# Kernel optimization log

Hardware: AMD Instinct MI355X
Metric: run time of the kernel (lower is better)

The kernel has to match this reference:

```python
import jax, jax.numpy as jnp
import numpy as np

ALPHA = 0.15  # init kwarg alpha


def setup_inputs() -> dict:
    key = jax.random.key(0)
    k1, k2, k3, k4 = jax.random.split(key, 4)
    B, H, W, C = 16, 1024, 1024, 1
    I1 = jax.random.normal(k1, (B, H, W, C), jnp.float32)
    I2 = jax.random.normal(k2, (B, H, W, C), jnp.float32)
    u = jax.random.normal(k3, (B, H, W, C), jnp.float32)
    v = jax.random.normal(k4, (B, H, W, C), jnp.float32)
    return {"I1": I1, "I2": I2, "u": u, "v": v}


def _image_gradients(img):
    # Matches tf.image.image_gradients: returns (dy, dx), with last row/col zero.
    B, H, W, C = img.shape
    dy = jnp.concatenate([img[:, 1:, :, :] - img[:, :-1, :, :],
                          jnp.zeros((B, 1, W, C), img.dtype)], axis=1)
    dx = jnp.concatenate([img[:, :, 1:, :] - img[:, :, :-1, :],
                          jnp.zeros((B, H, 1, C), img.dtype)], axis=2)
    return dy, dx


def _warp(img, u, v):
    # Bilinear warp with zero padding at sample coords (x + 0.5*u, y + 0.5*v).
    # (The [-1,1] normalization + grid_sample align-corners denorm is identity.)
    B, H, W, C = img.shape
    x = jnp.arange(W, dtype=img.dtype)[None, None, :] + 0.5 * u[..., 0]  # (B,H,W)
    y = jnp.arange(H, dtype=img.dtype)[None, :, None] + 0.5 * v[..., 0]  # (B,H,W)
    x0 = jnp.floor(x)
    y0 = jnp.floor(y)
    x1 = x0 + 1.0
    y1 = y0 + 1.0
    wx1 = x - x0
    wx0 = 1.0 - wx1
    wy1 = y - y0
    wy0 = 1.0 - wy1
    img_flat = img.reshape(B, H * W, C)

    def gather(yi, xi):
        valid = (xi >= 0) & (xi <= W - 1) & (yi >= 0) & (yi <= H - 1)
        xi_c = jnp.clip(xi, 0, W - 1).astype(jnp.int32)
        yi_c = jnp.clip(yi, 0, H - 1).astype(jnp.int32)
        idx = (yi_c * W + xi_c).reshape(B, H * W, 1)
        vals = jnp.take_along_axis(img_flat, idx, axis=1).reshape(B, H, W, C)
        return vals * valid[..., None].astype(img.dtype)

    out = (gather(y0, x0) * (wy0 * wx0)[..., None]
           + gather(y0, x1) * (wy0 * wx1)[..., None]
           + gather(y1, x0) * (wy1 * wx0)[..., None]
           + gather(y1, x1) * (wy1 * wx1)[..., None])
    return out


def reference(I1, I2, u, v):
    # NOTE: faithful to the source, which assigns grad_x, grad_y = image_gradients(.)
    # even though tf.image.image_gradients returns (dy, dx).
    I1_grad_x, I1_grad_y = _image_gradients(I1)
    I1_warped = _warp(I1, u, v)
    dataTerm = I1_warped - I2
    u_next = u - ALPHA * dataTerm * I1_grad_x
    v_next = v - ALPHA * dataTerm * I1_grad_y
    return (u_next, v_next)
```

## Files before the change

### kernel.cpp

```cpp
#include <hip/hip_runtime.h>


#define ALPHA 0.15f
#define IMG_H 1024
#define IMG_W 1024
#define TW 128
#define TH 8
#define HALO 4
#define LW (TW + 9)
#define LH (TH + 9)

typedef float f32x4 __attribute__((ext_vector_type(4)));

__global__ __launch_bounds__(256) void dataterm_kernel(
        const float* __restrict__ I1,
        const float* __restrict__ I2,
        const float* __restrict__ u,
        const float* __restrict__ v,
        float* __restrict__ out_u,
        float* __restrict__ out_v) {
    const int W = IMG_W, H = IMG_H;
    const int t   = threadIdx.x;
    const int tx0 = blockIdx.x * TW;
    const int ty0 = blockIdx.y * TH;
    const int b   = blockIdx.z;

    const float* __restrict__ I1b = I1 + (size_t)b * (size_t)(H * W);

    __shared__ float S[LH * LW];

    for (int f = t; f < LH * LW; f += 256) {
        int ly = f / LW;
        int lx = f - ly * LW;
        int gy = min(max(ty0 - HALO + ly, 0), H - 1);
        int gx = min(max(tx0 - HALO + lx, 0), W - 1);
        S[f] = I1b[gy * W + gx];
    }
    __syncthreads();

    const int r  = t >> 5;
    const int cb = (t & 31) << 2;
    const int h  = ty0 + r;
    const int wb = tx0 + cb;
    const int p  = (b * H + h) * W + wb;

    f32x4 u4  = *(const f32x4*)(u + p);
    f32x4 v4  = *(const f32x4*)(v + p);
    f32x4 i24 = *(const f32x4*)(I2 + p);

    float uu[4] = { u4.x, u4.y, u4.z, u4.w };
    float vv[4] = { v4.x, v4.y, v4.z, v4.w };
    float i2[4] = { i24.x, i24.y, i24.z, i24.w };
    float ru[4], rv[4];

    const int cl = (HALO + r) * LW + HALO + cb;

    #pragma unroll
    for (int i = 0; i < 4; ++i) {
        float c     = S[cl + i];
        float right = S[cl + i + 1];
        float down  = S[cl + i + LW];
        float gxv = right - c;
        float gyv = down - c;

        float x = (float)(wb + i) + 0.5f * uu[i];
        float y = (float)h        + 0.5f * vv[i];

        float x0f = floorf(x);
        float y0f = floorf(y);
        float wx1 = x - x0f;
        float wx0 = 1.0f - wx1;
        float wy1 = y - y0f;
        float wy0 = 1.0f - wy1;

        int x0 = (int)x0f, y0 = (int)y0f;
        int x1 = x0 + 1,   y1 = y0 + 1;

        float vx0 = (x0 >= 0 && x0 <= W - 1) ? 1.0f : 0.0f;
        float vx1 = (x1 >= 0 && x1 <= W - 1) ? 1.0f : 0.0f;
        float vy0 = (y0 >= 0 && y0 <= H - 1) ? 1.0f : 0.0f;
        float vy1 = (y1 >= 0 && y1 <= H - 1) ? 1.0f : 0.0f;

        int lx0 = x0 - tx0 + HALO;
        int ly0 = y0 - ty0 + HALO;

        float g00, g01, g10, g11;
        if ((unsigned)lx0 <= (unsigned)(LW - 2) &&
            (unsigned)ly0 <= (unsigned)(LH - 2)) {
            int q = ly0 * LW + lx0;
            g00 = S[q]          * (vy0 * vx0);
            g01 = S[q + 1]      * (vy0 * vx1);
            g10 = S[q + LW]     * (vy1 * vx0);
            g11 = S[q + LW + 1] * (vy1 * vx1);
        } else {
            int x0c = min(max(x0, 0), W - 1);
            int x1c = min(max(x1, 0), W - 1);
            int y0c = min(max(y0, 0), H - 1);
            int y1c = min(max(y1, 0), H - 1);
            g00 = I1b[y0c * W + x0c] * (vy0 * vx0);
            g01 = I1b[y0c * W + x1c] * (vy0 * vx1);
            g10 = I1b[y1c * W + x0c] * (vy1 * vx0);
            g11 = I1b[y1c * W + x1c] * (vy1 * vx1);
        }

        float warped = g00 * (wy0 * wx0)
                     + g01 * (wy0 * wx1)
                     + g10 * (wy1 * wx0)
                     + g11 * (wy1 * wx1);

        float dataTerm = warped - i2[i];
        ru[i] = uu[i] - ALPHA * dataTerm * gyv;
        rv[i] = vv[i] - ALPHA * dataTerm * gxv;
    }

    f32x4 ruv = { ru[0], ru[1], ru[2], ru[3] };
    f32x4 rvv = { rv[0], rv[1], rv[2], rv[3] };
    __builtin_nontemporal_store(ruv, (f32x4*)(out_u + p));
    __builtin_nontemporal_store(rvv, (f32x4*)(out_v + p));
}

extern "C" void kernel_launch(void* const* d_in, const int* in_sizes, int n_in,
                              void* d_out, int out_size, void* d_ws, size_t ws_size,
                              hipStream_t stream) {
    const float* I1 = (const float*)d_in[0];
    const float* I2 = (const float*)d_in[1];
    const float* u  = (const float*)d_in[2];
    const float* v  = (const float*)d_in[3];

    int total = in_sizes[0];
    float* out_u = (float*)d_out;
    float* out_v = (float*)d_out + total;

    dim3 grid(IMG_W / TW, IMG_H / TH, total / (IMG_H * IMG_W));
    dataterm_kernel<<<grid, dim3(256), 0, stream>>>(I1, I2, u, v, out_u, out_v);
}
```

Measured before the change: 70.71 us.

## Double tile height, load halo via global_load_lds, prefetch streams before staging

Result: slower. 78.99 us (+11.7%).

```diff
diff --git a/kernel.cpp b/kernel.cpp
--- a/kernel.cpp
+++ b/kernel.cpp
@@ -5,10 +5,11 @@
 #define IMG_H 1024
 #define IMG_W 1024
 #define TW 128
-#define TH 8
+#define TH 16
 #define HALO 4
-#define LW (TW + 9)
-#define LH (TH + 9)
+#define LW 140
+#define LH 25
+#define LDS_N 3584
 
 typedef float f32x4 __attribute__((ext_vector_type(4)));
 
@@ -27,96 +28,113 @@
 
     const float* __restrict__ I1b = I1 + (size_t)b * (size_t)(H * W);
 
-    __shared__ float S[LH * LW];
+    __shared__ float S[LDS_N];
 
-    for (int f = t; f < LH * LW; f += 256) {
+    const int r  = t >> 5;
+    const int cb = (t & 31) << 2;
+    const int h0 = ty0 + r;
+    const int wb = tx0 + cb;
+    const int p0 = (b * H + h0) * W + wb;
+    const int p1 = p0 + 8 * W;
+
+    f32x4 u4a = *(const f32x4*)(u + p0);
+    f32x4 v4a = *(const f32x4*)(v + p0);
+    f32x4 i2a = *(const f32x4*)(I2 + p0);
+    f32x4 u4b = *(const f32x4*)(u + p1);
+    f32x4 v4b = *(const f32x4*)(v + p1);
+    f32x4 i2b = *(const f32x4*)(I2 + p1);
+
+    #pragma unroll
+    for (int j = 0; j < 14; ++j) {
+        int f  = t + 256 * j;
         int ly = f / LW;
         int lx = f - ly * LW;
-        int gy = min(max(ty0 - HALO + ly, 0), H - 1);
+        int gy = min(max(ty0 - HALO + min(ly, LH - 1), 0), H - 1);
         int gx = min(max(tx0 - HALO + lx, 0), W - 1);
-        S[f] = I1b[gy * W + gx];
+        __builtin_amdgcn_global_load_lds(
+            (const __attribute__((address_space(1))) void*)(I1b + gy * W + gx),
+            (__attribute__((address_space(3))) void*)(S + f), 4, 0, 0);
     }
     __syncthreads();
 
-    const int r  = t >> 5;
-    const int cb = (t & 31) << 2;
-    const int h  = ty0 + r;
-    const int wb = tx0 + cb;
-    const int p  = (b * H + h) * W + wb;
+    float ou[8], ov[8];
 
-    f32x4 u4  = *(const f32x4*)(u + p);
-    f32x4 v4  = *(const f32x4*)(v + p);
-    f32x4 i24 = *(const f32x4*)(I2 + p);
+    auto proc4 = [&](int h, int cl, const f32x4& u4, const f32x4& v4,
+                     const f32x4& i24, float* ru, float* rv) {
+        f32x4 c4 = *(const f32x4*)(S + cl);
+        f32x4 d4 = *(const f32x4*)(S + cl + LW);
+        float c4r = S[cl + 4];
+        float gyv[4] = { d4.x - c4.x, d4.y - c4.y, d4.z - c4.z, d4.w - c4.w };
+        float gxv[4] = { c4.y - c4.x, c4.z - c4.y, c4.w - c4.z, c4r - c4.w };
+        float uu[4] = { u4.x, u4.y, u4.z, u4.w };
+        float vv[4] = { v4.x, v4.y, v4.z, v4.w };
+        float i2[4] = { i24.x, i24.y, i24.z, i24.w };
 
-    float uu[4] = { u4.x, u4.y, u4.z, u4.w };
-    float vv[4] = { v4.x, v4.y, v4.z, v4.w };
-    float i2[4] = { i24.x, i24.y, i24.z, i24.w };
-    float ru[4], rv[4];
+        #pragma unroll
+        for (int i = 0; i < 4; ++i) {
+            float x = (float)(wb + i) + 0.5f * uu[i];
+            float y = (float)h        + 0.5f * vv[i];
 
-    const int cl = (HALO + r) * LW + HALO + cb;
+            float x0f = floorf(x);
+            float y0f = floorf(y);
+            float wx1 = x - x0f;
+            float wx0 = 1.0f - wx1;
+            float wy1 = y - y0f;
+            float wy0 = 1.0f - wy1;
 
-    #pragma unroll
-    for (int i = 0; i < 4; ++i) {
-        float c     = S[cl + i];
-        float right = S[cl + i + 1];
-        float down  = S[cl + i + LW];
-        float gxv = right - c;
-        float gyv = down - c;
+            int x0 = (int)x0f, y0 = (int)y0f;
+            int x1 = x0 + 1,   y1 = y0 + 1;
 
-        float x = (float)(wb + i) + 0.5f * uu[i];
-        float y = (float)h        + 0.5f * vv[i];
+            float vx0 = (x0 >= 0 && x0 <= W - 1) ? 1.0f : 0.0f;
+            float vx1 = (x1 >= 0 && x1 <= W - 1) ? 1.0f : 0.0f;
+            float vy0 = (y0 >= 0 && y0 <= H - 1) ? 1.0f : 0.0f;
+            float vy1 = (y1 >= 0 && y1 <= H - 1) ? 1.0f : 0.0f;
 
-        float x0f = floorf(x);
-        float y0f = floorf(y);
-        float wx1 = x - x0f;
-        float wx0 = 1.0f - wx1;
-        float wy1 = y - y0f;
-        float wy0 = 1.0f - wy1;
+            int lx0 = x0 - tx0 + HALO;
+            int ly0 = y0 - ty0 + HALO;
 
-        int x0 = (int)x0f, y0 = (int)y0f;
-        int x1 = x0 + 1,   y1 = y0 + 1;
+            float g00, g01, g10, g11;
+            if ((unsigned)lx0 <= (unsigned)(LW - 2) &&
+                (unsigned)ly0 <= (unsigned)(LH - 2)) {
+                int q = ly0 * LW + lx0;
+                g00 = S[q]          * (vy0 * vx0);
+                g01 = S[q + 1]      * (vy0 * vx1);
+                g10 = S[q + LW]     * (vy1 * vx0);
+                g11 = S[q + LW + 1] * (vy1 * vx1);
+            } else {
+                int x0c = min(max(x0, 0), W - 1);
+                int x1c = min(max(x1, 0), W - 1);
+                int y0c = min(max(y0, 0), H - 1);
+                int y1c = min(max(y1, 0), H - 1);
+                g00 = I1b[y0c * W + x0c] * (vy0 * vx0);
+                g01 = I1b[y0c * W + x1c] * (vy0 * vx1);
+                g10 = I1b[y1c * W + x0c] * (vy1 * vx0);
+                g11 = I1b[y1c * W + x1c] * (vy1 * vx1);
+            }
 
-        float vx0 = (x0 >= 0 && x0 <= W - 1) ? 1.0f : 0.0f;
-        float vx1 = (x1 >= 0 && x1 <= W - 1) ? 1.0f : 0.0f;
-        float vy0 = (y0 >= 0 && y0 <= H - 1) ? 1.0f : 0.0f;
-        float vy1 = (y1 >= 0 && y1 <= H - 1) ? 1.0f : 0.0f;
+            float warped = g00 * (wy0 * wx0)
+                         + g01 * (wy0 * wx1)
+                         + g10 * (wy1 * wx0)
+                         + g11 * (wy1 * wx1);
 
-        int lx0 = x0 - tx0 + HALO;
-        int ly0 = y0 - ty0 + HALO;
+            float dataTerm = warped - i2[i];
+            ru[i] = uu[i] - ALPHA * dataTerm * gyv[i];
+            rv[i] = vv[i] - ALPHA * dataTerm * gxv[i];
+        }
+    };
 
-        float g00, g01, g10, g11;
-        if ((unsigned)lx0 <= (unsigned)(LW - 2) &&
-            (unsigned)ly0 <= (unsigned)(LH - 2)) {
-            int q = ly0 * LW + lx0;
-            g00 = S[q]          * (vy0 * vx0);
-            g01 = S[q + 1]      * (vy0 * vx1);
-            g10 = S[q + LW]     * (vy1 * vx0);
-            g11 = S[q + LW + 1] * (vy1 * vx1);
-        } else {
-            int x0c = min(max(x0, 0), W - 1);
-            int x1c = min(max(x1, 0), W - 1);
-            int y0c = min(max(y0, 0), H - 1);
-            int y1c = min(max(y1, 0), H - 1);
-            g00 = I1b[y0c * W + x0c] * (vy0 * vx0);
-            g01 = I1b[y0c * W + x1c] * (vy0 * vx1);
-            g10 = I1b[y1c * W + x0c] * (vy1 * vx0);
-            g11 = I1b[y1c * W + x1c] * (vy1 * vx1);
-        }
+    const int clA = (HALO + r) * LW + HALO + cb;
+    proc4(h0,     clA,            u4a, v4a, i2a, ou,     ov);
+    proc4(h0 + 8, clA + 8 * LW,   u4b, v4b, i2b, ou + 4, ov + 4);
 
-        float warped = g00 * (wy0 * wx0)
-                     + g01 * (wy0 * wx1)
-                     + g10 * (wy1 * wx0)
-                     + g11 * (wy1 * wx1);
-
-        float dataTerm = warped - i2[i];
-        ru[i] = uu[i] - ALPHA * dataTerm * gyv;
-        rv[i] = vv[i] - ALPHA * dataTerm * gxv;
-    }
-
-    f32x4 ruv = { ru[0], ru[1], ru[2], ru[3] };
-    f32x4 rvv = { rv[0], rv[1], rv[2], rv[3] };
-    __builtin_nontemporal_store(ruv, (f32x4*)(out_u + p));
-    __builtin_nontemporal_store(rvv, (f32x4*)(out_v + p));
+    f32x4 ruA = { ou[0], ou[1], ou[2], ou[3] };
+    f32x4 rvA = { ov[0], ov[1], ov[2], ov[3] };
+    f32x4 ruB = { ou[4], ou[5], ou[6], ou[7] };
+    f32x4 rvB = { ov[4], ov[5], ov[6], ov[7] };
+    __builtin_nontemporal_store(ruA, (f32x4*)(out_u + p0));
+    __builtin_nontemporal_store(rvA, (f32x4*)(out_v + p0));
+    __builtin_nontemporal_store(ruB, (f32x4*)(out_u + p1));
+    __builtin_nontemporal_store(rvB, (f32x4*)(out_v + p1));
 }
 
 extern "C" void kernel_launch(void* const* d_in, const int* in_sizes, int n_in,
```
